# Kernel tuning notes

Hardware: AMD Instinct MI355X
Metric: run time of the kernel (lower is better)

The kernel has to match this reference:

```python
import jax, jax.numpy as jnp
import numpy as np

D = 1024
M = 16
H = D // M  # 64
EPS = 1e-05


def setup_inputs() -> dict:
    key = jax.random.key(0)
    ks = jax.random.split(key, 5)
    B, T = 4, 1024
    x = jax.random.normal(ks[0], (B, T, D), dtype=jnp.float32)
    norm_w = jnp.ones((D,), dtype=jnp.float32)
    s = 1.0 / np.sqrt(D)
    W_v = jax.random.uniform(ks[1], (D, D), dtype=jnp.float32, minval=-s, maxval=s)
    W_a = jax.random.uniform(ks[2], (H * M * (M + 1), D), dtype=jnp.float32, minval=-s, maxval=s)
    W_out = jax.random.uniform(ks[3], (D, D), dtype=jnp.float32, minval=-s, maxval=s)
    return {"x": x, "norm_w": norm_w, "W_v": W_v, "W_a": W_a, "W_out": W_out}


def _rmsnorm(x, w, eps=EPS):
    var = jnp.mean(jnp.square(x), axis=-1, keepdims=True)
    return x * jax.lax.rsqrt(var + eps) * w


def reference(x, norm_w, W_v, W_a, W_out):
    B, T, _ = x.shape
    h = _rmsnorm(x, norm_w)                              # [B,T,D]
    v = (h @ W_v.T).reshape(B, T, H, M)                  # [B,T,H,m]
    gate_logits = (h @ W_a.T).reshape(B, T, H, M, M + 1)
    gates = jax.nn.softmax(gate_logits, axis=-1)
    a0 = gates[..., 0]                                   # [B,T,H,m]
    A = gates[..., 1:]                                   # [B,T,H,m,m]

    # time-major for scan
    A_t = jnp.moveaxis(A, 1, 0)                          # [T,B,H,m,m]
    u_t = jnp.moveaxis(a0 * v, 1, 0)                     # [T,B,H,m]

    def step(state, inp):
        At, ut = inp
        new = jnp.einsum('bhij,bhj->bhi', At, state) + ut
        return new, new

    init = jnp.zeros((B, H, M), dtype=x.dtype)
    _, ys = jax.lax.scan(step, init, (A_t, u_t))         # ys: [T,B,H,m]
    h_out = jnp.moveaxis(ys, 0, 1).reshape(B, T, D)
    return x + h_out @ W_out.T
```

## Files before the change

### kernel.cpp

```cpp
#include <hip/hip_runtime.h>
#include <hip/hip_bf16.h>
#include <math.h>

#define B_DIM 4
#define T_DIM 1024
#define D_DIM 1024
#define M_DIM 16
#define H_DIM 64
#define NT    4096
#define NA    17408
#define NCAT  18432
#define EPSV  1e-5f
#define CL    16
#define NC    64

typedef __bf16 bf16_t;
typedef __bf16 bf16x4 __attribute__((ext_vector_type(4)));
typedef __bf16 bf16x8 __attribute__((ext_vector_type(8)));
typedef float  f32x4  __attribute__((ext_vector_type(4)));

#define PBAR() do { asm volatile("" ::: "memory"); __builtin_amdgcn_s_barrier(); asm volatile("" ::: "memory"); } while (0)

__global__ __launch_bounds__(256) void cvt_all_kernel(const float* __restrict__ Wa,
                                                      const float* __restrict__ Wv,
                                                      const float* __restrict__ Wo,
                                                      bf16_t* __restrict__ wcat,
                                                      bf16_t* __restrict__ wo) {
  constexpr int NA4 = NA * D_DIM / 4;
  constexpr int NV4 = D_DIM * D_DIM / 4;
  constexpr int total = NA4 + 2 * NV4;
  int idx = blockIdx.x * blockDim.x + threadIdx.x;
  int stride = gridDim.x * blockDim.x;
  for (; idx < total; idx += stride) {
    const float* src; bf16_t* dst; int j;
    if (idx < NA4)            { src = Wa; dst = wcat; j = idx; }
    else if (idx < NA4 + NV4) { src = Wv; dst = wcat + (size_t)NA * D_DIM; j = idx - NA4; }
    else                      { src = Wo; dst = wo; j = idx - NA4 - NV4; }
    float4 v = reinterpret_cast<const float4*>(src)[j];
    bf16x4 o;
    o[0] = (bf16_t)v.x; o[1] = (bf16_t)v.y; o[2] = (bf16_t)v.z; o[3] = (bf16_t)v.w;
    reinterpret_cast<bf16x4*>(dst)[j] = o;
  }
}

__global__ __launch_bounds__(256) void rmsnorm_kernel(const float* __restrict__ x,
                                                      const float* __restrict__ w,
                                                      bf16_t* __restrict__ h) {
  int row = blockIdx.x;
  int tid = threadIdx.x;
  const float4* xr = reinterpret_cast<const float4*>(x + (size_t)row * D_DIM);
  float4 xv = xr[tid];
  float ss = xv.x * xv.x + xv.y * xv.y + xv.z * xv.z + xv.w * xv.w;
#pragma unroll
  for (int m = 1; m < 64; m <<= 1) ss += __shfl_xor(ss, m, 64);
  __shared__ float red[4];
  int lane = tid & 63, wid = tid >> 6;
  if (lane == 0) red[wid] = ss;
  __syncthreads();
  float tot = red[0] + red[1] + red[2] + red[3];
  float scale = rsqrtf(tot * (1.0f / D_DIM) + EPSV);
  float4 wv = reinterpret_cast<const float4*>(w)[tid];
  bf16x4 o;
  o[0] = (bf16_t)(xv.x * scale * wv.x);
  o[1] = (bf16_t)(xv.y * scale * wv.y);
  o[2] = (bf16_t)(xv.z * scale * wv.z);
  o[3] = (bf16_t)(xv.w * scale * wv.w);
  reinterpret_cast<bf16x4*>(h)[(size_t)row * 256 + tid] = o;
}

__global__ __launch_bounds__(256) void gemm_out_kernel(const bf16_t* __restrict__ A,
                                                       const bf16_t* __restrict__ Bw,
                                                       float* __restrict__ Cout,
                                                       const float* __restrict__ resid,
                                                       int Ndim, int K) {
  constexpr int BM = 128, BN = 128, BK = 32;
  __shared__ bf16_t As[BM * BK];
  __shared__ bf16_t Bs[BN * BK];

  int tid = threadIdx.x;
  int lane = tid & 63;
  int wid = tid >> 6;
  int wm = wid >> 1, wn = wid & 1;
  int bm = blockIdx.x * BM;
  int bn = blockIdx.y * BN;
  int l15 = lane & 15;
  int l4 = lane >> 4;

  f32x4 acc[4][4];
#pragma unroll
  for (int i = 0; i < 4; i++)
#pragma unroll
    for (int j = 0; j < 4; j++) acc[i][j] = (f32x4){0.f, 0.f, 0.f, 0.f};

  const bf16_t* Ag = A + (size_t)bm * K;
  const bf16_t* Bg = Bw + (size_t)bn * K;
  int srow_lane = lane >> 2;
  int scol = (lane & 3) * 8;

  for (int k0 = 0; k0 < K; k0 += BK) {
#pragma unroll
    for (int i = 0; i < 2; i++) {
      int rbase = wid * 32 + i * 16;
      int r = rbase + srow_lane;
      __builtin_amdgcn_global_load_lds(
          (const __attribute__((address_space(1))) void*)(Ag + (size_t)r * K + k0 + scol),
          (__attribute__((address_space(3))) void*)(As + rbase * BK), 16, 0, 0);
      __builtin_amdgcn_global_load_lds(
          (const __attribute__((address_space(1))) void*)(Bg + (size_t)r * K + k0 + scol),
          (__attribute__((address_space(3))) void*)(Bs + rbase * BK), 16, 0, 0);
    }
    __syncthreads();

    const bf16x8* Asv = reinterpret_cast<const bf16x8*>(As);
    const bf16x8* Bsv = reinterpret_cast<const bf16x8*>(Bs);
    bf16x8 af[4], bfr[4];
#pragma unroll
    for (int mf = 0; mf < 4; mf++)
      af[mf] = Asv[(wm * 64 + mf * 16 + l15) * 4 + l4];
#pragma unroll
    for (int nf = 0; nf < 4; nf++)
      bfr[nf] = Bsv[(wn * 64 + nf * 16 + l15) * 4 + l4];
#pragma unroll
    for (int mf = 0; mf < 4; mf++)
#pragma unroll
      for (int nf = 0; nf < 4; nf++)
        acc[mf][nf] = __builtin_amdgcn_mfma_f32_16x16x32_bf16(af[mf], bfr[nf], acc[mf][nf], 0, 0, 0);
    __syncthreads();
  }

#pragma unroll
  for (int mf = 0; mf < 4; mf++)
#pragma unroll
    for (int nf = 0; nf < 4; nf++)
#pragma unroll
      for (int i = 0; i < 4; i++) {
        int row = bm + wm * 64 + mf * 16 + l4 * 4 + i;
        int col = bn + wn * 64 + nf * 16 + l15;
        size_t idx = (size_t)row * Ndim + col;
        Cout[idx] = acc[mf][nf][i] + resid[idx];
      }
}

__global__ __launch_bounds__(512, 2) void gemm256_nt_kernel(const bf16_t* __restrict__ A,
                                                            const bf16_t* __restrict__ Bw,
                                                            bf16_t* __restrict__ Clg,
                                                            float* __restrict__ Cv) {
  constexpr int K = 1024;
  constexpr int G = K / 64;
  __shared__ bf16_t As[2 * 16384];
  __shared__ bf16_t Bs[2 * 16384];

  const int tid = threadIdx.x;
  const int lane = tid & 63;
  const int w = tid >> 6;
  const int wm = w >> 2;
  const int wn = w & 3;
  const int l15 = lane & 15;
  const int l4 = lane >> 4;

  const int bm = blockIdx.x * 256;
  const int bn = blockIdx.y * 256;

  const bf16_t* Ag = A + (size_t)bm * K;
  const bf16_t* Bg = Bw + (size_t)bn * K;

  int growi[2], gcoli[2];
#pragma unroll
  for (int j = 0; j < 2; ++j) {
    int E = j * 4096 + tid * 8;
    int sub = E >> 9, e = E & 511;
    int rin = e >> 5, cs = e & 31;
    int cin = cs ^ ((rin & 8) ? 16 : 0);
    growi[j] = (sub >> 1) * 16 + rin;
    gcoli[j] = (sub & 1) * 32 + cin;
  }

  const int fbase = l15 * 32 + ((l4 * 8) ^ ((l15 & 8) ? 16 : 0));

  f32x4 acc[8][4];
#pragma unroll
  for (int i = 0; i < 8; i++)
#pragma unroll
    for (int j = 0; j < 4; j++) acc[i][j] = (f32x4){0.f, 0.f, 0.f, 0.f};

  bf16x8 ALo[8], AHi[8], B0r[4], B1r[4];

  auto stageHalf = [&](const bf16_t* Gp, bf16_t* Lp, int bufp, int half, int t2) {
#pragma unroll
    for (int j = 0; j < 2; ++j) {
      const bf16_t* src = Gp + (size_t)(half * 128 + growi[j]) * K + t2 * 64 + gcoli[j];
      __builtin_amdgcn_global_load_lds(
          (const __attribute__((address_space(1))) void*)src,
          (__attribute__((address_space(3))) void*)(Lp + bufp * 16384 + half * 8192 + j * 4096 + w * 512),
          16, 0, 0);
    }
  };

  auto rdA4 = [&](bf16x8* dst, int bufp, int rgrpBase) {
    const bf16_t* base = As + bufp * 16384;
#pragma unroll
    for (int mf = 0; mf < 4; ++mf)
#pragma unroll
      for (int kk = 0; kk < 2; ++kk)
        dst[mf * 2 + kk] = *reinterpret_cast<const bf16x8*>(base + ((rgrpBase + mf) * 2 + kk) * 512 + fbase);
  };
  auto rdA2 = [&](bf16x8* dst, int bufp, int rgrpBase) {
    const bf16_t* base = As + bufp * 16384;
#pragma unroll
    for (int mf = 0; mf < 2; ++mf)
#pragma unroll
      for (int kk = 0; kk < 2; ++kk)
        dst[mf * 2 + kk] = *reinterpret_cast<const bf16x8*>(base + ((rgrpBase + mf) * 2 + kk) * 512 + fbase);
  };
  auto rdB = [&](bf16x8* dst, int bufp, int nfBase) {
    const bf16_t* base = Bs + bufp * 16384;
#pragma unroll
    for (int nf = 0; nf < 2; ++nf)
#pragma unroll
      for (int kk = 0; kk < 2; ++kk)
        dst[nf * 2 + kk] = *reinterpret_cast<const bf16x8*>(base + ((wn * 4 + nfBase + nf) * 2 + kk) * 512 + fbase);
  };
  auto MM = [&](const bf16x8* Af, const bf16x8* Bf, int mfB, int nfB) {
    __builtin_amdgcn_s_setprio(1);
#pragma unroll
    for (int mf = 0; mf < 4; ++mf)
#pragma unroll
      for (int nf = 0; nf < 2; ++nf)
#pragma unroll
        for (int kk = 0; kk < 2; ++kk)
          acc[mfB + mf][nfB + nf] = __builtin_amdgcn_mfma_f32_16x16x32_bf16(
              Af[mf * 2 + kk], Bf[nf * 2 + kk], acc[mfB + mf][nfB + nf], 0, 0, 0);
    __builtin_amdgcn_s_setprio(0);
  };

  stageHalf(Bg, Bs, 0, 0, 0);
  stageHalf(Bg, Bs, 0, 1, 0);
  stageHalf(Ag, As, 0, 0, 0);
  stageHalf(Ag, As, 0, 1, 0);
  stageHalf(Ag, As, 1, 0, 1);
  stageHalf(Ag, As, 1, 1, 1);
  asm volatile("s_waitcnt vmcnt(0)" ::: "memory");
  PBAR();
  rdA4(ALo, 0, wm * 8);

#pragma unroll 1
  for (int t = 0; t < G; ++t) {
    const int buf = t & 1;
    const int nbuf = buf ^ 1;

    rdB(B0r, buf, 0);
    rdA2(AHi, buf, wm * 8 + 4);
    if (t + 1 < G) stageHalf(Bg, Bs, nbuf, 0, t + 1);
    PBAR();
    MM(ALo, B0r, 0, 0);
    PBAR();

    rdB(B1r, buf, 2);
    rdA2(AHi + 4, buf, wm * 8 + 6);
    if (t + 1 < G) stageHalf(Bg, Bs, nbuf, 1, t + 1);
    PBAR();
    MM(ALo, B1r, 0, 2);
    if (t + 1 < G) asm volatile("s_waitcnt vmcnt(4)" ::: "memory");
    PBAR();

    if (t + 1 < G) rdA4(ALo, nbuf, wm * 8);
    if (t + 2 < G) stageHalf(Ag, As, buf, 0, t + 2);
    PBAR();
    MM(AHi, B0r, 4, 0);
    PBAR();

    if (t + 2 < G) stageHalf(Ag, As, buf, 1, t + 2);
    PBAR();
    MM(AHi, B1r, 4, 2);
    if (t + 2 < G)      asm volatile("s_waitcnt vmcnt(4)" ::: "memory");
    else if (t + 1 < G) asm volatile("s_waitcnt vmcnt(0)" ::: "memory");
    PBAR();
  }

  if (blockIdx.y < 68) {
#pragma unroll
    for (int mf = 0; mf < 8; ++mf)
#pragma unroll
      for (int nf = 0; nf < 4; ++nf)
#pragma unroll
        for (int i = 0; i < 4; ++i) {
          int row = bm + wm * 128 + mf * 16 + l4 * 4 + i;
          int col = bn + wn * 64 + nf * 16 + l15;
          Clg[(size_t)row * NA + col] = (bf16_t)acc[mf][nf][i];
        }
  } else {
    int cb = bn - NA;
#pragma unroll
    for (int mf = 0; mf < 8; ++mf)
#pragma unroll
      for (int nf = 0; nf < 4; ++nf)
#pragma unroll
        for (int i = 0; i < 4; ++i) {
          int row = bm + wm * 128 + mf * 16 + l4 * 4 + i;
          int col = cb + wn * 64 + nf * 16 + l15;
          Cv[(size_t)row * D_DIM + col] = acc[mf][nf][i];
        }
  }
}

__device__ __forceinline__ void softmax17(const bf16_t* __restrict__ lp, float vval,
                                          f32x4& a0, f32x4& a1, f32x4& a2, f32x4& a3,
                                          float& u) {
  float e[17];
  float mx = -1e30f;
#pragma unroll
  for (int j = 0; j < 17; ++j) {
    e[j] = (float)lp[j];
    mx = fmaxf(mx, e[j]);
  }
  float s = 0.f;
#pragma unroll
  for (int j = 0; j < 17; ++j) {
    e[j] = __expf(e[j] - mx);
    s += e[j];
  }
  float inv = 1.0f / s;
  a0 = (f32x4){e[1] * inv, e[2] * inv, e[3] * inv, e[4] * inv};
  a1 = (f32x4){e[5] * inv, e[6] * inv, e[7] * inv, e[8] * inv};
  a2 = (f32x4){e[9] * inv, e[10] * inv, e[11] * inv, e[12] * inv};
  a3 = (f32x4){e[13] * inv, e[14] * inv, e[15] * inv, e[16] * inv};
  u = e[0] * inv * vval;
}

__global__ __launch_bounds__(256) void scanA_kernel(const bf16_t* __restrict__ lg,
                                                    const float* __restrict__ v,
                                                    float* __restrict__ sum) {
  int bc = blockIdx.x;
  int b = bc >> 6;
  int c = bc & 63;
  int g = threadIdx.x >> 4;
  int i = threadIdx.x & 15;
  int h = blockIdx.y * 16 + g;
  int chain = b * 64 + h;

  __shared__ float Arows[16][16][16];
  __shared__ float Us[16][16];

  f32x4 R0 = (f32x4){i == 0 ? 1.f : 0.f, i == 1 ? 1.f : 0.f, i == 2 ? 1.f : 0.f, i == 3 ? 1.f : 0.f};
  f32x4 R1 = (f32x4){i == 4 ? 1.f : 0.f, i == 5 ? 1.f : 0.f, i == 6 ? 1.f : 0.f, i == 7 ? 1.f : 0.f};
  f32x4 R2 = (f32x4){i == 8 ? 1.f : 0.f, i == 9 ? 1.f : 0.f, i == 10 ? 1.f : 0.f, i == 11 ? 1.f : 0.f};
  f32x4 R3 = (f32x4){i == 12 ? 1.f : 0.f, i == 13 ? 1.f : 0.f, i == 14 ? 1.f : 0.f, i == 15 ? 1.f : 0.f};
  float q = 0.f;

#pragma unroll 1
  for (int tau = CL - 1; tau >= 0; --tau) {
    int r = b * T_DIM + c * CL + tau;
    const bf16_t* lp = lg + (size_t)r * NA + h * 272 + i * 17;
    float vval = v[(size_t)r * D_DIM + h * 16 + i];
    f32x4 a0, a1, a2, a3;
    float uu;
    softmax17(lp, vval, a0, a1, a2, a3, uu);

    *reinterpret_cast<f32x4*>(&Arows[g][i][0]) = a0;
    *reinterpret_cast<f32x4*>(&Arows[g][i][4]) = a1;
    *reinterpret_cast<f32x4*>(&Arows[g][i][8]) = a2;
    *reinterpret_cast<f32x4*>(&Arows[g][i][12]) = a3;
    Us[g][i] = uu;
    asm volatile("s_waitcnt lgkmcnt(0)" ::: "memory");
    __builtin_amdgcn_sched_barrier(0);

    f32x4 u0 = *reinterpret_cast<const f32x4*>(&Us[g][0]);
    f32x4 u1 = *reinterpret_cast<const f32x4*>(&Us[g][4]);
    f32x4 u2 = *reinterpret_cast<const f32x4*>(&Us[g][8]);
    f32x4 u3 = *reinterpret_cast<const f32x4*>(&Us[g][12]);
    float qa = fmaf(R0[0], u0[0], fmaf(R0[1], u0[1], fmaf(R0[2], u0[2], R0[3] * u0[3])));
    float qb = fmaf(R1[0], u1[0], fmaf(R1[1], u1[1], fmaf(R1[2], u1[2], R1[3] * u1[3])));
    float qc = fmaf(R2[0], u2[0], fmaf(R2[1], u2[1], fmaf(R2[2], u2[2], R2[3] * u2[3])));
    float qd = fmaf(R3[0], u3[0], fmaf(R3[1], u3[1], fmaf(R3[2], u3[2], R3[3] * u3[3])));
    q += (qa + qb) + (qc + qd);

    f32x4 n0 = (f32x4){0.f, 0.f, 0.f, 0.f}, n1 = n0, n2 = n0, n3 = n0;
#pragma unroll
    for (int k = 0; k < 16; ++k) {
      float rk = (k < 4) ? R0[k & 3] : (k < 8) ? R1[k & 3] : (k < 12) ? R2[k & 3] : R3[k & 3];
      f32x4 b0 = *reinterpret_cast<const f32x4*>(&Arows[g][k][0]);
      f32x4 b1 = *reinterpret_cast<const f32x4*>(&Arows[g][k][4]);
      f32x4 b2 = *reinterpret_cast<const f32x4*>(&Arows[g][k][8]);
      f32x4 b3 = *reinterpret_cast<const f32x4*>(&Arows[g][k][12]);
#pragma unroll
      for (int e2 = 0; e2 < 4; ++e2) {
        n0[e2] = fmaf(rk, b0[e2], n0[e2]);
        n1[e2] = fmaf(rk, b1[e2], n1[e2]);
        n2[e2] = fmaf(rk, b2[e2], n2[e2]);
        n3[e2] = fmaf(rk, b3[e2], n3[e2]);
      }
    }
    R0 = n0; R1 = n1; R2 = n2; R3 = n3;
  }

  float* sp = sum + (size_t)(chain * NC + c) * 272;
  *reinterpret_cast<f32x4*>(&sp[i * 16 + 0]) = R0;
  *reinterpret_cast<f32x4*>(&sp[i * 16 + 4]) = R1;
  *reinterpret_cast<f32x4*>(&sp[i * 16 + 8]) = R2;
  *reinterpret_cast<f32x4*>(&sp[i * 16 + 12]) = R3;
  sp[256 + i] = q;
}

__global__ __launch_bounds__(64) void scanB_kernel(const float* __restrict__ sum,
                                                   float* __restrict__ sinit) {
  int chain = blockIdx.x;
  int lane = threadIdx.x;
  int i = lane & 15;

  __shared__ float seg[2][2176];

  const float* gbase = sum + (size_t)chain * NC * 272;

  auto load_seg = [&](int s, int buf) {
#pragma unroll
    for (int r = 0; r < 9; ++r) {
      int idx = r * 256 + lane * 4;
      if (idx < 2176) {
        __builtin_amdgcn_global_load_lds(
            (const __attribute__((address_space(1))) void*)(gbase + (size_t)s * 2176 + idx),
            (__attribute__((address_space(3))) void*)(&seg[buf][r * 256]), 16, 0, 0);
      }
    }
  };

  load_seg(0, 0);
  asm volatile("s_waitcnt vmcnt(0)" ::: "memory");
  __builtin_amdgcn_sched_barrier(0);

  f32x4 S0 = (f32x4){0.f, 0.f, 0.f, 0.f}, S1 = S0, S2 = S0, S3 = S0;
  float own = 0.f;

  for (int sg = 0; sg < 8; ++sg) {
    int buf = sg & 1;
    if (sg + 1 < 8) load_seg(sg + 1, buf ^ 1);
#pragma unroll 1
    for (int cc = 0; cc < 8; ++cc) {
      int c = sg * 8 + cc;
      const float* Pb = &seg[buf][cc * 272];
      if (lane < 16) sinit[(size_t)(chain * NC + c) * 16 + i] = own;

      f32x4 p0 = *reinterpret_cast<const f32x4*>(&Pb[i * 16 + 0]);
      f32x4 p1 = *reinterpret_cast<const f32x4*>(&Pb[i * 16 + 4]);
      f32x4 p2 = *reinterpret_cast<const f32x4*>(&Pb[i * 16 + 8]);
      f32x4 p3 = *reinterpret_cast<const f32x4*>(&Pb[i * 16 + 12]);
      float qq = Pb[256 + i];

      float pa = fmaf(p0[0], S0[0], fmaf(p0[1], S0[1], fmaf(p0[2], S0[2], p0[3] * S0[3])));
      float pb = fmaf(p1[0], S1[0], fmaf(p1[1], S1[1], fmaf(p1[2], S1[2], p1[3] * S1[3])));
      float pc = fmaf(p2[0], S2[0], fmaf(p2[1], S2[1], fmaf(p2[2], S2[2], p2[3] * S2[3])));
      float pd = fmaf(p3[0], S3[0], fmaf(p3[1], S3[1], fmaf(p3[2], S3[2], p3[3] * S3[3])));
      float p = (pa + pb) + (pc + pd) + qq;
      own = p;

#pragma unroll
      for (int j = 0; j < 4; ++j) {
        S0[j] = __shfl(p, j, 64);
        S1[j] = __shfl(p, 4 + j, 64);
        S2[j] = __shfl(p, 8 + j, 64);
        S3[j] = __shfl(p, 12 + j, 64);
      }
    }
    if (sg + 1 < 8) {
      asm volatile("s_waitcnt vmcnt(0)" ::: "memory");
      __builtin_amdgcn_sched_barrier(0);
    }
  }
}

__global__ __launch_bounds__(256) void scanC_kernel(const bf16_t* __restrict__ lg,
                                                    const float* __restrict__ v,
                                                    const float* __restrict__ sinit,
                                                    bf16_t* __restrict__ y) {
  int bc = blockIdx.x;
  int b = bc >> 6;
  int c = bc & 63;
  int g = threadIdx.x >> 4;
  int i = threadIdx.x & 15;
  int h = blockIdx.y * 16 + g;
  int chain = b * 64 + h;

  __shared__ float Sb[16][16];

  const float* ip = sinit + (size_t)(chain * NC + c) * 16;
  f32x4 S0 = *reinterpret_cast<const f32x4*>(&ip[0]);
  f32x4 S1 = *reinterpret_cast<const f32x4*>(&ip[4]);
  f32x4 S2 = *reinterpret_cast<const f32x4*>(&ip[8]);
  f32x4 S3 = *reinterpret_cast<const f32x4*>(&ip[12]);

#pragma unroll 1
  for (int t = 0; t < CL; ++t) {
    int r = b * T_DIM + c * CL + t;
    const bf16_t* lp = lg + (size_t)r * NA + h * 272 + i * 17;
    float vval = v[(size_t)r * D_DIM + h * 16 + i];
    f32x4 a0, a1, a2, a3;
    float uu;
    softmax17(lp, vval, a0, a1, a2, a3, uu);

    float pa = fmaf(a0[0], S0[0], fmaf(a0[1], S0[1], fmaf(a0[2], S0[2], a0[3] * S0[3])));
    float pb = fmaf(a1[0], S1[0], fmaf(a1[1], S1[1], fmaf(a1[2], S1[2], a1[3] * S1[3])));
    float pc = fmaf(a2[0], S2[0], fmaf(a2[1], S2[1], fmaf(a2[2], S2[2], a2[3] * S2[3])));
    float pd = fmaf(a3[0], S3[0], fmaf(a3[1], S3[1], fmaf(a3[2], S3[2], a3[3] * S3[3])));
    float p = (pa + pb) + (pc + pd) + uu;

    y[(size_t)r * D_DIM + h * 16 + i] = (bf16_t)p;

    Sb[g][i] = p;
    asm volatile("s_waitcnt lgkmcnt(0)" ::: "memory");
    __builtin_amdgcn_sched_barrier(0);
    S0 = *reinterpret_cast<const f32x4*>(&Sb[g][0]);
    S1 = *reinterpret_cast<const f32x4*>(&Sb[g][4]);
    S2 = *reinterpret_cast<const f32x4*>(&Sb[g][8]);
    S3 = *reinterpret_cast<const f32x4*>(&Sb[g][12]);
  }
}

extern "C" void kernel_launch(void* const* d_in, const int* in_sizes, int n_in,
                              void* d_out, int out_size, void* d_ws, size_t ws_size,
                              hipStream_t stream) {
  const float* x      = (const float*)d_in[0];
  const float* norm_w = (const float*)d_in[1];
  const float* W_v    = (const float*)d_in[2];
  const float* W_a    = (const float*)d_in[3];
  const float* W_out  = (const float*)d_in[4];

  char* ws = (char*)d_ws;
  size_t off = 0;
  auto alloc = [&](size_t bytes) {
    void* p = ws + off;
    off += (bytes + 255) & ~(size_t)255;
    return p;
  };
  bf16_t* wcat = (bf16_t*)alloc((size_t)NCAT * D_DIM * 2);
  bf16_t* wo_b = (bf16_t*)alloc((size_t)D_DIM * D_DIM * 2);
  bf16_t* h_b  = (bf16_t*)alloc((size_t)NT * D_DIM * 2);
  float*  v_f  = (float*)alloc((size_t)NT * D_DIM * 4);
  bf16_t* lg_b = (bf16_t*)alloc((size_t)NT * NA * 2);
  bf16_t* y_b  = (bf16_t*)alloc((size_t)NT * D_DIM * 2);
  float*  sum_f   = (float*)alloc((size_t)256 * NC * 272 * 4);
  float*  sinit_f = (float*)alloc((size_t)256 * NC * 16 * 4);

  cvt_all_kernel<<<2048, 256, 0, stream>>>(W_a, W_v, W_out, wcat, wo_b);

  rmsnorm_kernel<<<NT, 256, 0, stream>>>(x, norm_w, h_b);

  gemm256_nt_kernel<<<dim3(NT / 256, NCAT / 256), 512, 0, stream>>>(h_b, wcat, lg_b, v_f);

  scanA_kernel<<<dim3(256, 4), 256, 0, stream>>>(lg_b, v_f, sum_f);
  scanB_kernel<<<256, 64, 0, stream>>>(sum_f, sinit_f);
  scanC_kernel<<<dim3(256, 4), 256, 0, stream>>>(lg_b, v_f, sinit_f, y_b);

  gemm_out_kernel<<<dim3(NT / 128, D_DIM / 128), 256, 0, stream>>>(
      y_b, wo_b, (float*)d_out, x, D_DIM, D_DIM);
}
```

Before: 334.6 us.

## Fuse weight conversion with rmsnorm and permute gate weights for coalesced scan loads

Merges the weight fp32->bf16 conversion and rmsnorm into a single launch, cutting one kernel launch. The conversion also permutes W_a rows within each head so that logit j of row i sits at column j*16+i, not i*17+j. The scan kernels then read the 17 logits with a stride of 16 elements, so the 16 threads of a group read adjacent addresses instead of scattered 17-element strides. This adds integer div/mod index math to the conversion and depends on the GEMM output layout following the permuted weight order.

Result: no change. 337.3 us (+0.8%).

```diff
diff --git a/kernel.cpp b/kernel.cpp
--- a/kernel.cpp
+++ b/kernel.cpp
@@ -18,54 +18,68 @@
 typedef __bf16 bf16x4 __attribute__((ext_vector_type(4)));
 typedef __bf16 bf16x8 __attribute__((ext_vector_type(8)));
 typedef float  f32x4  __attribute__((ext_vector_type(4)));
+typedef unsigned short u16;
 
 #define PBAR() do { asm volatile("" ::: "memory"); __builtin_amdgcn_s_barrier(); asm volatile("" ::: "memory"); } while (0)
-
-__global__ __launch_bounds__(256) void cvt_all_kernel(const float* __restrict__ Wa,
-                                                      const float* __restrict__ Wv,
-                                                      const float* __restrict__ Wo,
-                                                      bf16_t* __restrict__ wcat,
-                                                      bf16_t* __restrict__ wo) {
-  constexpr int NA4 = NA * D_DIM / 4;
-  constexpr int NV4 = D_DIM * D_DIM / 4;
-  constexpr int total = NA4 + 2 * NV4;
-  int idx = blockIdx.x * blockDim.x + threadIdx.x;
-  int stride = gridDim.x * blockDim.x;
-  for (; idx < total; idx += stride) {
-    const float* src; bf16_t* dst; int j;
-    if (idx < NA4)            { src = Wa; dst = wcat; j = idx; }
-    else if (idx < NA4 + NV4) { src = Wv; dst = wcat + (size_t)NA * D_DIM; j = idx - NA4; }
-    else                      { src = Wo; dst = wo; j = idx - NA4 - NV4; }
-    float4 v = reinterpret_cast<const float4*>(src)[j];
+#define VM0()   do { asm volatile("s_waitcnt vmcnt(0)" ::: "memory"); __builtin_amdgcn_sched_barrier(0); } while (0)
+
+__global__ __launch_bounds__(256) void prep_kernel(const float* __restrict__ x,
+                                                   const float* __restrict__ nw,
+                                                   const float* __restrict__ Wa,
+                                                   const float* __restrict__ Wv,
+                                                   const float* __restrict__ Wo,
+                                                   bf16_t* __restrict__ h,
+                                                   bf16_t* __restrict__ wcat,
+                                                   bf16_t* __restrict__ wo) {
+  int tid = threadIdx.x;
+  if (blockIdx.x < NT) {
+    int row = blockIdx.x;
+    const float4* xr = reinterpret_cast<const float4*>(x + (size_t)row * D_DIM);
+    float4 xv = xr[tid];
+    float ss = xv.x * xv.x + xv.y * xv.y + xv.z * xv.z + xv.w * xv.w;
+#pragma unroll
+    for (int m = 1; m < 64; m <<= 1) ss += __shfl_xor(ss, m, 64);
+    __shared__ float red[4];
+    int lane = tid & 63, wid = tid >> 6;
+    if (lane == 0) red[wid] = ss;
+    __syncthreads();
+    float tot = red[0] + red[1] + red[2] + red[3];
+    float scale = rsqrtf(tot * (1.0f / D_DIM) + EPSV);
+    float4 wv = reinterpret_cast<const float4*>(nw)[tid];
     bf16x4 o;
-    o[0] = (bf16_t)v.x; o[1] = (bf16_t)v.y; o[2] = (bf16_t)v.z; o[3] = (bf16_t)v.w;
-    reinterpret_cast<bf16x4*>(dst)[j] = o;
-  }
-}
-
-__global__ __launch_bounds__(256) void rmsnorm_kernel(const float* __restrict__ x,
-                                                      const float* __restrict__ w,
-                                                      bf16_t* __restrict__ h) {
-  int row = blockIdx.x;
-  int tid = threadIdx.x;
-  const float4* xr = reinterpret_cast<const float4*>(x + (size_t)row * D_DIM);
-  float4 xv = xr[tid];
-  float ss = xv.x * xv.x + xv.y * xv.y + xv.z * xv.z + xv.w * xv.w;
-#pragma unroll
-  for (int m = 1; m < 64; m <<= 1) ss += __shfl_xor(ss, m, 64);
-  __shared__ float red[4];
-  int lane = tid & 63, wid = tid >> 6;
-  if (lane == 0) red[wid] = ss;
-  __syncthreads();
-  float tot = red[0] + red[1] + red[2] + red[3];
-  float scale = rsqrtf(tot * (1.0f / D_DIM) + EPSV);
-  float4 wv = reinterpret_cast<const float4*>(w)[tid];
-  bf16x4 o;
-  o[0] = (bf16_t)(xv.x * scale * wv.x);
-  o[1] = (bf16_t)(xv.y * scale * wv.y);
-  o[2] = (bf16_t)(xv.z * scale * wv.z);
-  o[3] = (bf16_t)(xv.w * scale * wv.w);
-  reinterpret_cast<bf16x4*>(h)[(size_t)row * 256 + tid] = o;
+    o[0] = (bf16_t)(xv.x * scale * wv.x);
+    o[1] = (bf16_t)(xv.y * scale * wv.y);
+    o[2] = (bf16_t)(xv.z * scale * wv.z);
+    o[3] = (bf16_t)(xv.w * scale * wv.w);
+    reinterpret_cast<bf16x4*>(h)[(size_t)row * 256 + tid] = o;
+  } else {
+    constexpr int NA4 = NA * D_DIM / 4;
+    constexpr int NV4 = D_DIM * D_DIM / 4;
+    constexpr int total = NA4 + 2 * NV4;
+    int nb = gridDim.x - NT;
+    int idx = (blockIdx.x - NT) * 256 + tid;
+    int stride = nb * 256;
+    for (; idx < total; idx += stride) {
+      const float* src; bf16_t* dst; int js, jd;
+      if (idx < NA4) {
+        src = Wa; dst = wcat; js = idx;
+        int row = idx >> 8;
+        int c4 = idx & 255;
+        int hh = row / 272, r = row - hh * 272;
+        int ii = r / 17, jj = r - ii * 17;
+        int nrow = hh * 272 + jj * 16 + ii;
+        jd = (nrow << 8) + c4;
+      } else if (idx < NA4 + NV4) {
+        src = Wv; dst = wcat + (size_t)NA * D_DIM; js = idx - NA4; jd = js;
+      } else {
+        src = Wo; dst = wo; js = idx - NA4 - NV4; jd = js;
+      }
+      float4 v = reinterpret_cast<const float4*>(src)[js];
+      bf16x4 o;
+      o[0] = (bf16_t)v.x; o[1] = (bf16_t)v.y; o[2] = (bf16_t)v.z; o[3] = (bf16_t)v.w;
+      reinterpret_cast<bf16x4*>(dst)[jd] = o;
+    }
+  }
 }
 
 __global__ __launch_bounds__(256) void gemm_out_kernel(const bf16_t* __restrict__ A,
@@ -303,14 +317,15 @@
   }
 }
 
-__device__ __forceinline__ void softmax17(const bf16_t* __restrict__ lp, float vval,
-                                          f32x4& a0, f32x4& a1, f32x4& a2, f32x4& a3,
-                                          float& u) {
+__device__ __forceinline__ void softmax17s(const bf16_t* __restrict__ bp, float vval,
+                                           f32x4& a0, f32x4& a1, f32x4& a2, f32x4& a3,
+                                           float& u) {
+  const u16* lp = reinterpret_cast<const u16*>(bp);
   float e[17];
   float mx = -1e30f;
 #pragma unroll
   for (int j = 0; j < 17; ++j) {
-    e[j] = (float)lp[j];
+    e[j] = __uint_as_float(((unsigned)lp[j * 16]) << 16);
     mx = fmaxf(mx, e[j]);
   }
   float s = 0.f;
@@ -337,6 +352,7 @@
   int i = threadIdx.x & 15;
   int h = blockIdx.y * 16 + g;
   int chain = b * 64 + h;
+  int rbase = b * T_DIM + c * CL;
 
   __shared__ float Arows[16][16][16];
   __shared__ float Us[16][16];
@@ -349,12 +365,11 @@
 
 #pragma unroll 1
   for (int tau = CL - 1; tau >= 0; --tau) {
-    int r = b * T_DIM + c * CL + tau;
-    const bf16_t* lp = lg + (size_t)r * NA + h * 272 + i * 17;
+    int r = rbase + tau;
     float vval = v[(size_t)r * D_DIM + h * 16 + i];
     f32x4 a0, a1, a2, a3;
     float uu;
-    softmax17(lp, vval, a0, a1, a2, a3, uu);
+    softmax17s(lg + (size_t)r * NA + h * 272 + i, vval, a0, a1, a2, a3, uu);
 
     *reinterpret_cast<f32x4*>(&Arows[g][i][0]) = a0;
     *reinterpret_cast<f32x4*>(&Arows[g][i][4]) = a1;
@@ -424,8 +439,7 @@
   };
 
   load_seg(0, 0);
-  asm volatile("s_waitcnt vmcnt(0)" ::: "memory");
-  __builtin_amdgcn_sched_barrier(0);
+  VM0();
 
   f32x4 S0 = (f32x4){0.f, 0.f, 0.f, 0.f}, S1 = S0, S2 = S0, S3 = S0;
   float own = 0.f;
@@ -460,10 +474,7 @@
         S3[j] = __shfl(p, 12 + j, 64);
       }
     }
-    if (sg + 1 < 8) {
-      asm volatile("s_waitcnt vmcnt(0)" ::: "memory");
-      __builtin_amdgcn_sched_barrier(0);
-    }
+    if (sg + 1 < 8) VM0();
   }
 }
 
@@ -478,6 +489,7 @@
   int i = threadIdx.x & 15;
   int h = blockIdx.y * 16 + g;
   int chain = b * 64 + h;
+  int rbase = b * T_DIM + c * CL;
 
   __shared__ float Sb[16][16];
 
@@ -489,12 +501,11 @@
 
 #pragma unroll 1
   for (int t = 0; t < CL; ++t) {
-    int r = b * T_DIM + c * CL + t;
-    const bf16_t* lp = lg + (size_t)r * NA + h * 272 + i * 17;
+    int r = rbase + t;
     float vval = v[(size_t)r * D_DIM + h * 16 + i];
     f32x4 a0, a1, a2, a3;
     float uu;
-    softmax17(lp, vval, a0, a1, a2, a3, uu);
+    softmax17s(lg + (size_t)r * NA + h * 272 + i, vval, a0, a1, a2, a3, uu);
 
     float pa = fmaf(a0[0], S0[0], fmaf(a0[1], S0[1], fmaf(a0[2], S0[2], a0[3] * S0[3])));
     float pb = fmaf(a1[0], S1[0], fmaf(a1[1], S1[1], fmaf(a1[2], S1[2], a1[3] * S1[3])));
@@ -539,9 +550,8 @@
   float*  sum_f   = (float*)alloc((size_t)256 * NC * 272 * 4);
   float*  sinit_f = (float*)alloc((size_t)256 * NC * 16 * 4);
 
-  cvt_all_kernel<<<2048, 256, 0, stream>>>(W_a, W_v, W_out, wcat, wo_b);
-
-  rmsnorm_kernel<<<NT, 256, 0, stream>>>(x, norm_w, h_b);
+  prep_kernel<<<NT + 2048, 256, 0, stream>>>(x, norm_w, W_a, W_v, W_out,
+                                             h_b, wcat, wo_b);
 
   gemm256_nt_kernel<<<dim3(NT / 256, NCAT / 256), 512, 0, stream>>>(h_b, wcat, lg_b, v_f);
 
```
